# Kernel optimization log

Hardware: AMD Instinct MI355X
Metric: run time of the kernel (lower is better)

Reference implementation:

```python
import jax, jax.numpy as jnp
import numpy as np

B, S, D, H, DK, DV = 2, 2048, 1024, 16, 64, 64


def setup_inputs() -> dict:
    key = jax.random.key(0)
    ks = jax.random.split(key, 12)
    inp = {
        "query": jax.random.normal(ks[0], (B, S, D), jnp.float32),
        "key":   jax.random.normal(ks[1], (B, S, D), jnp.float32),
        "value": jax.random.normal(ks[2], (B, S, D), jnp.float32),
        # additive mask broadcast over per-head [B,S,S] scores (zeros = no masking)
        "mask":  jnp.zeros((S, S), jnp.float32),
        # stacked per-head projection params (math-equivalent to H separate Linears)
        "Wq": jax.random.normal(ks[3], (H, D, DK), jnp.float32) / np.sqrt(D),
        "bq": jax.random.normal(ks[4], (H, DK), jnp.float32) * 0.02,
        "Wk": jax.random.normal(ks[5], (H, D, DK), jnp.float32) / np.sqrt(D),
        "bk": jax.random.normal(ks[6], (H, DK), jnp.float32) * 0.02,
        "Wv": jax.random.normal(ks[7], (H, D, DV), jnp.float32) / np.sqrt(D),
        "bv": jax.random.normal(ks[8], (H, DV), jnp.float32) * 0.02,
        "Wo": jax.random.normal(ks[9], (H * DV, D), jnp.float32) / np.sqrt(H * DV),
        "bo": jax.random.normal(ks[10], (D,), jnp.float32) * 0.02,
    }
    return inp


def reference(query, key, value, mask, Wq, bq, Wk, bk, Wv, bv, Wo, bo):
    # per-head projections, vectorized over heads
    q = jnp.einsum("bsd,hdk->bhsk", query, Wq) + bq[None, :, None, :]
    k = jnp.einsum("bsd,hdk->bhsk", key, Wk) + bk[None, :, None, :]
    v = jnp.einsum("bsd,hdv->bhsv", value, Wv) + bv[None, :, None, :]
    # explicit QK^T softmax V, scale by sqrt(dim_k) (key.size(-1))
    scores = jnp.einsum("bhsk,bhtk->bhst", q, k) / jnp.sqrt(jnp.asarray(DK, q.dtype))
    scores = scores + mask  # broadcast [S,S] -> [B,H,S,S]
    attn = jax.nn.softmax(scores, axis=-1)
    out = jnp.einsum("bhst,bhtv->bhsv", attn, v)
    # concat heads along last dim: [B,S,H*DV]
    out = out.transpose(0, 2, 1, 3).reshape(B, S, H * DV)
    return out @ Wo + bo
```

## Files before the change

kernel.cpp:

```cpp
#include <hip/hip_runtime.h>
#include <stdint.h>

typedef __bf16 bf16;
typedef float f32x4 __attribute__((ext_vector_type(4)));
typedef __bf16 bf16x8 __attribute__((ext_vector_type(8)));
typedef __bf16 bf16x4 __attribute__((ext_vector_type(4)));

__device__ __forceinline__ void async_load16(const void* g, void* l) {
    __builtin_amdgcn_global_load_lds(
        (const __attribute__((address_space(1))) void*)g,
        (__attribute__((address_space(3))) void*)l, 16, 0, 0);
}

__global__ void detect_dtype(const unsigned short* __restrict__ q, int* __restrict__ flag) {
    __shared__ int cnt;
    if (threadIdx.x == 0) cnt = 0;
    __syncthreads();
    int c = 0;
    for (int i = threadIdx.x; i < 4096; i += 256) {
        int e = (q[i] >> 7) & 0xFF;
        if (e >= 0xC0) ++c;
    }
    atomicAdd(&cnt, c);
    __syncthreads();
    if (threadIdx.x == 0) { flag[0] = (cnt > 64) ? 1 : 0; flag[1] = 0; }
}

__global__ void prep(const void* __restrict__ qv, const void* __restrict__ vv,
                     const void* __restrict__ wq, const void* __restrict__ wk,
                     const void* __restrict__ wv, const void* __restrict__ wo,
                     const unsigned int* __restrict__ mask,
                     bf16* __restrict__ Xq, bf16* __restrict__ Xv,
                     bf16* __restrict__ WqT, bf16* __restrict__ WoT,
                     int* __restrict__ flag) {
    __shared__ bf16 t[32][33];
    const int f    = flag[0];
    const int task = blockIdx.z;
    const int bid  = blockIdx.x + 64 * blockIdx.y;

    if (task < 2) {
        const void* x = task ? vv : qv;
        bf16* o = task ? Xv : Xq;
        size_t i = ((size_t)bid * 256 + threadIdx.x) * 8;
        if (f) {
            f32x4 a = ((const f32x4*)x)[i / 4];
            f32x4 b = ((const f32x4*)x)[i / 4 + 1];
            bf16x8 v;
            for (int j = 0; j < 4; ++j) { v[j] = (bf16)a[j]; v[4 + j] = (bf16)b[j]; }
            *(bf16x8*)(o + i) = v;
        } else {
            *(bf16x8*)(o + i) = *(const bf16x8*)((const bf16*)x + i);
        }
    } else if (task < 5) {
        if (bid >= 1024) return;
        const void* in = (task == 2) ? wq : ((task == 3) ? wk : wv);
        int sub = bid >> 6, rem = bid & 63;
        int c0 = (rem & 1) * 32, r0 = (rem >> 1) * 32;
        int tx = threadIdx.x & 31, ty = threadIdx.x >> 5;
        size_t base = (size_t)sub * 65536;
        if (f) {
            const float* inF = (const float*)in;
            for (int i = 0; i < 32; i += 8)
                t[ty + i][tx] = (bf16)inF[base + (size_t)(r0 + ty + i) * 64 + (c0 + tx)];
        } else {
            const bf16* inB = (const bf16*)in;
            for (int i = 0; i < 32; i += 8)
                t[ty + i][tx] = inB[base + (size_t)(r0 + ty + i) * 64 + (c0 + tx)];
        }
        __syncthreads();
        bf16* o = WqT + ((size_t)(task - 2) * 16 + sub) * 65536;
        for (int i = 0; i < 32; i += 8)
            o[(size_t)(c0 + ty + i) * 1024 + (r0 + tx)] = t[tx][ty + i];
    } else if (task == 5) {
        if (bid >= 1024) return;
        int c0 = (bid & 31) * 32, r0 = (bid >> 5) * 32;
        int tx = threadIdx.x & 31, ty = threadIdx.x >> 5;
        if (f) {
            const float* inF = (const float*)wo;
            for (int i = 0; i < 32; i += 8)
                t[ty + i][tx] = (bf16)inF[(size_t)(r0 + ty + i) * 1024 + (c0 + tx)];
        } else {
            const bf16* inB = (const bf16*)wo;
            for (int i = 0; i < 32; i += 8)
                t[ty + i][tx] = inB[(size_t)(r0 + ty + i) * 1024 + (c0 + tx)];
        }
        __syncthreads();
        for (int i = 0; i < 32; i += 8)
            WoT[(size_t)(c0 + ty + i) * 1024 + (r0 + tx)] = t[tx][ty + i];
    } else {
        const long nvec = (f ? 4194304L : 2097152L) / 4;
        unsigned int acc = 0;
        long stride = 2048L * 256;
        for (long i = (long)bid * 256 + threadIdx.x; i < nvec; i += stride) {
            uint4 v = ((const uint4*)mask)[i];
            acc |= v.x | v.y | v.z | v.w;
        }
        if (acc) atomicOr(flag + 1, 1);
    }
}

__global__ __launch_bounds__(256, 3) void gemm_qkv(
    const bf16* __restrict__ Xq, const void* __restrict__ keyRaw,
    const bf16* __restrict__ Xv, const bf16* __restrict__ Bt,
    const void* __restrict__ b0, const void* __restrict__ b1, const void* __restrict__ b2,
    bf16* __restrict__ Qp, bf16* __restrict__ Kp, bf16* __restrict__ Vt,
    const int* __restrict__ flag) {
    __shared__ __attribute__((aligned(16))) unsigned char AsRaw[128 * 64 * 4];
    __shared__ __attribute__((aligned(16))) bf16 Bs[128 * 64];

    const int f = flag[0];
    const int K = 1024, N = 1024;
    const int z = blockIdx.z;
    const int af = (z == 1) ? f : 0;
    const void* Av   = (z == 0) ? (const void*)Xq : ((z == 1) ? keyRaw : (const void*)Xv);
    const void* bias = (z == 0) ? b0 : ((z == 1) ? b1 : b2);
    const bf16* B    = Bt + (size_t)z * 1024 * 1024;

    const int tid  = threadIdx.x;
    const int lane = tid & 63;
    const int w    = tid >> 6;
    const int quad = lane >> 4;
    const int mrow = lane & 15;
    const int m0 = blockIdx.y * 128;
    const int n0 = blockIdx.x * 128;
    const int wm = (w & 1) * 64;
    const int wn = (w >> 1) * 64;

    f32x4 acc[4][4] = {};

    for (int k0 = 0; k0 < K; k0 += 64) {
        if (af) {
            for (int it = 0; it < 8; ++it) {
                int ci  = it * 256 + tid;
                int row = ci >> 4, pc = ci & 15;
                int swz = ((row & 7) << 1) | ((row >> 3) & 1);
                int gc  = pc ^ swz;
                async_load16((const float*)Av + (size_t)(m0 + row) * K + k0 + gc * 4,
                             AsRaw + (size_t)(it * 256 + w * 64) * 16);
            }
        } else {
            for (int it = 0; it < 4; ++it) {
                int ci  = it * 256 + tid;
                int row = ci >> 3, pc = ci & 7;
                int gc  = pc ^ (row & 7);
                async_load16((const bf16*)Av + (size_t)(m0 + row) * K + k0 + gc * 8,
                             (bf16*)AsRaw + (size_t)(it * 256 + w * 64) * 8);
            }
        }
        for (int it = 0; it < 4; ++it) {
            int ci  = it * 256 + tid;
            int row = ci >> 3, pc = ci & 7;
            int gc  = pc ^ (row & 7);
            async_load16(B + (size_t)(n0 + row) * K + k0 + gc * 8,
                         Bs + (size_t)(it * 256 + w * 64) * 8);
        }
        __syncthreads();
        for (int kk = 0; kk < 2; ++kk) {
            bf16x8 afr[4], bfr[4];
            if (af) {
                const float* Asf = (const float*)AsRaw;
                for (int mi = 0; mi < 4; ++mi) {
                    int row = wm + mi * 16 + mrow;
                    int swz = ((row & 7) << 1) | ((row >> 3) & 1);
                    int lc  = (kk * 4 + quad) * 2;
                    f32x4 u0 = *(const f32x4*)(Asf + row * 64 + (lc ^ swz) * 4);
                    f32x4 u1 = *(const f32x4*)(Asf + row * 64 + ((lc + 1) ^ swz) * 4);
                    for (int j = 0; j < 4; ++j) {
                        afr[mi][j]     = (bf16)u0[j];
                        afr[mi][4 + j] = (bf16)u1[j];
                    }
                }
            } else {
                const bf16* Asb = (const bf16*)AsRaw;
                for (int mi = 0; mi < 4; ++mi) {
                    int row = wm + mi * 16 + mrow;
                    int pc  = (kk * 4 + quad) ^ (row & 7);
                    afr[mi] = *(const bf16x8*)(Asb + row * 64 + pc * 8);
                }
            }
            for (int ni = 0; ni < 4; ++ni) {
                int row = wn + ni * 16 + mrow;
                int pc  = (kk * 4 + quad) ^ (row & 7);
                bfr[ni] = *(const bf16x8*)(Bs + row * 64 + pc * 8);
            }
            for (int mi = 0; mi < 4; ++mi)
                for (int ni = 0; ni < 4; ++ni)
                    acc[mi][ni] = __builtin_amdgcn_mfma_f32_16x16x32_bf16(
                        afr[mi], bfr[ni], acc[mi][ni], 0, 0, 0);
        }
        __syncthreads();
    }

    const float scl = (z == 0) ? 0.18033688f : 1.0f;
    for (int ni = 0; ni < 4; ++ni) {
        int n    = n0 + wn + ni * 16 + mrow;
        float bv = f ? ((const float*)bias)[n] : (float)((const bf16*)bias)[n];
        for (int mi = 0; mi < 4; ++mi) {
            int mb = m0 + wm + mi * 16 + quad * 4;
            if (z == 2) {
                bf16x4 pk;
                for (int r = 0; r < 4; ++r) pk[r] = (bf16)(acc[mi][ni][r] + bv);
                *(bf16x4*)(Vt + (((size_t)(mb >> 11) * 1024 + n) << 11) + (mb & 2047)) = pk;
            } else {
                bf16* P = (z == 0) ? Qp : Kp;
                for (int r = 0; r < 4; ++r)
                    P[(size_t)(mb + r) * N + n] = (bf16)((acc[mi][ni][r] + bv) * scl);
            }
        }
    }
}

__global__ __launch_bounds__(256, 2) void gemm_out(
    const bf16* __restrict__ A, const bf16* __restrict__ Bt,
    const void* __restrict__ bias, void* __restrict__ Cout,
    const int* __restrict__ flag) {
    __shared__ __attribute__((aligned(16))) bf16 As[128 * 64];
    __shared__ __attribute__((aligned(16))) bf16 Bs[64 * 64];

    const int f = flag[0];
    const int K = 1024, N = 1024;
    const int tid  = threadIdx.x;
    const int lane = tid & 63;
    const int w    = tid >> 6;
    const int quad = lane >> 4;
    const int mrow = lane & 15;
    const int m0 = blockIdx.y * 128;
    const int n0 = blockIdx.x * 64;
    const int wm = (w & 1) * 64;
    const int wn = (w >> 1) * 32;

    f32x4 acc[4][2] = {};

    for (int k0 = 0; k0 < K; k0 += 64) {
        for (int it = 0; it < 4; ++it) {
            int ci  = it * 256 + tid;
            int row = ci >> 3, pc = ci & 7;
            int gc  = pc ^ (row & 7);
            async_load16(A + (size_t)(m0 + row) * K + k0 + gc * 8,
                         As + (size_t)(it * 256 + w * 64) * 8);
        }
        for (int it = 0; it < 2; ++it) {
            int ci  = it * 256 + tid;
            int row = ci >> 3, pc = ci & 7;
            int gc  = pc ^ (row & 7);
            async_load16(Bt + (size_t)(n0 + row) * K + k0 + gc * 8,
                         Bs + (size_t)(it * 256 + w * 64) * 8);
        }
        __syncthreads();
        for (int kk = 0; kk < 2; ++kk) {
            bf16x8 afr[4], bfr[2];
            for (int mi = 0; mi < 4; ++mi) {
                int row = wm + mi * 16 + mrow;
                int pc  = (kk * 4 + quad) ^ (row & 7);
                afr[mi] = *(const bf16x8*)(As + row * 64 + pc * 8);
            }
            for (int ni = 0; ni < 2; ++ni) {
                int row = wn + ni * 16 + mrow;
                int pc  = (kk * 4 + quad) ^ (row & 7);
                bfr[ni] = *(const bf16x8*)(Bs + row * 64 + pc * 8);
            }
            for (int mi = 0; mi < 4; ++mi)
                for (int ni = 0; ni < 2; ++ni)
                    acc[mi][ni] = __builtin_amdgcn_mfma_f32_16x16x32_bf16(
                        afr[mi], bfr[ni], acc[mi][ni], 0, 0, 0);
        }
        __syncthreads();
    }

    for (int ni = 0; ni < 2; ++ni) {
        int n    = n0 + wn + ni * 16 + mrow;
        float bv = f ? ((const float*)bias)[n] : (float)((const bf16*)bias)[n];
        for (int mi = 0; mi < 4; ++mi) {
            int mb = m0 + wm + mi * 16 + quad * 4;
            for (int r = 0; r < 4; ++r) {
                float val = acc[mi][ni][r] + bv;
                if (f) ((float*)Cout)[(size_t)(mb + r) * N + n] = val;
                else   ((bf16*)Cout)[(size_t)(mb + r) * N + n] = (bf16)val;
            }
        }
    }
}

__global__ __launch_bounds__(256, 2) void flash_attn(
    const bf16* __restrict__ Qp, const bf16* __restrict__ Kp,
    const bf16* __restrict__ Vt, const void* __restrict__ maskv,
    bf16* __restrict__ O, const int* __restrict__ flag) {
    __shared__ __attribute__((aligned(16))) bf16 Ks[2][4096];
    __shared__ __attribute__((aligned(16))) bf16 Vs[2][4096];
    __shared__ __attribute__((aligned(16))) bf16 Ps[128 * 72];

    const int f       = flag[0];
    const int useMask = flag[1];
    const int tid  = threadIdx.x;
    const int lane = tid & 63;
    const int w    = tid >> 6;
    const int quad = lane >> 4;
    const int c    = lane & 15;
    const int s0   = blockIdx.x * 128;
    const int h    = blockIdx.y;
    const int b    = blockIdx.z;

    const size_t qkBase = (size_t)b * 2048 * 1024 + h * 64;
    const size_t vtBase = ((size_t)b * 1024 + h * 64) * 2048;

    const int ci0 = tid, ci1 = 256 + tid;
    const int r0 = ci0 >> 3, g0 = (ci0 & 7) ^ (r0 & 7);
    const int r1 = ci1 >> 3, g1 = (ci1 & 7) ^ (r1 & 7);
    const bf16* kp0 = Kp + qkBase + (size_t)r0 * 1024 + g0 * 8;
    const bf16* kp1 = Kp + qkBase + (size_t)r1 * 1024 + g1 * 8;
    const bf16* vp0 = Vt + vtBase + (size_t)r0 * 2048 + g0 * 8;
    const bf16* vp1 = Vt + vtBase + (size_t)r1 * 2048 + g1 * 8;

#define STAGE(B_, T_) do {                                                             \
        async_load16(kp0 + (size_t)(T_) * 1024, &Ks[B_][(size_t)(w * 64) * 8]);        \
        async_load16(kp1 + (size_t)(T_) * 1024, &Ks[B_][(size_t)(256 + w * 64) * 8]);  \
        async_load16(vp0 + (T_),                &Vs[B_][(size_t)(w * 64) * 8]);        \
        async_load16(vp1 + (T_),                &Vs[B_][(size_t)(256 + w * 64) * 8]);  \
    } while (0)

    const bf16* kf0 = &Ks[0][c * 64 + ((0 + quad) ^ (c & 7)) * 8];
    const bf16* kf1 = &Ks[0][c * 64 + ((4 + quad) ^ (c & 7)) * 8];
    const bf16* vf0 = &Vs[0][c * 64 + ((0 + quad) ^ (c & 7)) * 8];
    const bf16* vf1 = &Vs[0][c * 64 + ((4 + quad) ^ (c & 7)) * 8];
    bf16*       pw0 = Ps + (w * 32 + c) * 72 + quad * 4;
    bf16*       pw1 = Ps + (w * 32 + 16 + c) * 72 + quad * 4;
    const bf16* pr0 = Ps + (w * 32 + c) * 72 + quad * 8;
    const bf16* pr1 = Ps + (w * 32 + 16 + c) * 72 + quad * 8;

    bf16x8 aq[2][2];
    for (int hh = 0; hh < 2; ++hh) {
        const bf16* qrow = Qp + qkBase + (size_t)(s0 + w * 32 + hh * 16 + c) * 1024;
        aq[hh][0] = *(const bf16x8*)(qrow + quad * 8);
        aq[hh][1] = *(const bf16x8*)(qrow + 32 + quad * 8);
    }

    f32x4 o_acc[2][4] = {};
    float l_s[2] = {0.f, 0.f};

    const size_t mb0 = (size_t)(s0 + w * 32 + c) * 2048;
    const size_t mb1 = (size_t)(s0 + w * 32 + 16 + c) * 2048;

#define FCOMP(IB_, T_) do {                                                              \
        f32x4 sc[2][4] = {};                                                             \
        _Pragma("unroll") for (int tt = 0; tt < 4; ++tt) {                               \
            bf16x8 ak0 = *(const bf16x8*)(kf0 + (IB_) * 4096 + tt * 1024);               \
            bf16x8 ak1 = *(const bf16x8*)(kf1 + (IB_) * 4096 + tt * 1024);               \
            sc[0][tt] = __builtin_amdgcn_mfma_f32_16x16x32_bf16(ak0, aq[0][0], sc[0][tt], 0, 0, 0); \
            sc[0][tt] = __builtin_amdgcn_mfma_f32_16x16x32_bf16(ak1, aq[0][1], sc[0][tt], 0, 0, 0); \
            sc[1][tt] = __builtin_amdgcn_mfma_f32_16x16x32_bf16(ak0, aq[1][0], sc[1][tt], 0, 0, 0); \
            sc[1][tt] = __builtin_amdgcn_mfma_f32_16x16x32_bf16(ak1, aq[1][1], sc[1][tt], 0, 0, 0); \
        }                                                                                \
        if (useMask) {                                                                   \
            _Pragma("unroll") for (int hh = 0; hh < 2; ++hh) {                           \
                const size_t mr = (hh ? mb1 : mb0) + (T_);                               \
                _Pragma("unroll") for (int tt = 0; tt < 4; ++tt) {                       \
                    if (f) {                                                             \
                        f32x4 mk = *(const f32x4*)((const float*)maskv + mr + tt * 16 + quad * 4); \
                        for (int r = 0; r < 4; ++r) sc[hh][tt][r] += mk[r] * 1.44269504f; \
                    } else {                                                             \
                        bf16x4 mk = *(const bf16x4*)((const bf16*)maskv + mr + tt * 16 + quad * 4); \
                        for (int r = 0; r < 4; ++r) sc[hh][tt][r] += (float)mk[r] * 1.44269504f; \
                    }                                                                    \
                }                                                                        \
            }                                                                            \
        }                                                                                \
        _Pragma("unroll") for (int hh = 0; hh < 2; ++hh) {                               \
            float rsum = 0.f;                                                            \
            bf16* pw = hh ? pw1 : pw0;                                                   \
            _Pragma("unroll") for (int tt = 0; tt < 4; ++tt) {                           \
                bf16x4 pk;                                                               \
                for (int r = 0; r < 4; ++r) {                                            \
                    float p = exp2f(sc[hh][tt][r]);                                      \
                    rsum += p;                                                           \
                    pk[r] = (bf16)p;                                                     \
                }                                                                        \
                *(bf16x4*)(pw + tt * 16) = pk;                                           \
            }                                                                            \
            l_s[hh] += rsum;                                                             \
        }                                                                                \
        _Pragma("unroll") for (int kk = 0; kk < 2; ++kk) {                               \
            bf16x8 ap0 = *(const bf16x8*)((kk ? pr0 + 32 : pr0));                        \
            bf16x8 ap1 = *(const bf16x8*)((kk ? pr1 + 32 : pr1));                        \
            const bf16* vfb = kk ? vf1 : vf0;                                            \
            _Pragma("unroll") for (int ni = 0; ni < 4; ++ni) {                           \
                bf16x8 bv = *(const bf16x8*)(vfb + (IB_) * 4096 + ni * 1024);            \
                o_acc[0][ni] = __builtin_amdgcn_mfma_f32_16x16x32_bf16(ap0, bv, o_acc[0][ni], 0, 0, 0); \
                o_acc[1][ni] = __builtin_amdgcn_mfma_f32_16x16x32_bf16(ap1, bv, o_acc[1][ni], 0, 0, 0); \
            }                                                                            \
        }                                                                                \
    } while (0)

    STAGE(0, 0);
    for (int t0 = 0; t0 < 2048; t0 += 128) {
        __syncthreads();
        STAGE(1, t0 + 64);
        FCOMP(0, t0);
        __syncthreads();
        if (t0 + 128 < 2048) STAGE(0, t0 + 128);
        FCOMP(1, t0 + 64);
    }
#undef STAGE
#undef FCOMP

    for (int hh = 0; hh < 2; ++hh) {
        float ls = l_s[hh];
        ls += __shfl_xor(ls, 16, 64);
        ls += __shfl_xor(ls, 32, 64);
        for (int r = 0; r < 4; ++r) {
            float lv   = __shfl(ls, quad * 4 + r, 64);
            float inv  = 1.0f / lv;
            size_t roff = (size_t)(b * 2048 + s0 + w * 32 + hh * 16 + quad * 4 + r) * 1024 + h * 64;
            for (int ni = 0; ni < 4; ++ni)
                O[roff + ni * 16 + c] = (bf16)(o_acc[hh][ni][r] * inv);
        }
    }
}

extern "C" void kernel_launch(void* const* d_in, const int* in_sizes, int n_in,
                              void* d_out, int out_size, void* d_ws, size_t ws_size,
                              hipStream_t stream) {
    bf16* ws = (bf16*)d_ws;
    (void)in_sizes; (void)n_in; (void)out_size; (void)ws_size;

    const size_t MM = 1024 * 1024;
    int*  flag = (int*)ws;
    bf16* WqT  = ws + 8;
    bf16* WoT  = WqT + 3 * MM;
    bf16* Qp   = WoT + MM;
    bf16* Kp   = Qp + 4 * MM;
    bf16* Xq   = Kp + 4 * MM;
    bf16* AO   = Xq;
    bf16* Xv   = (bf16*)d_out;
    bf16* Vt   = (bf16*)d_out + 4 * MM;

    detect_dtype<<<1, 256, 0, stream>>>((const unsigned short*)d_in[0], flag);

    prep<<<dim3(64, 32, 7), 256, 0, stream>>>(d_in[0], d_in[2], d_in[4], d_in[6],
                                              d_in[8], d_in[10],
                                              (const unsigned int*)d_in[3],
                                              Xq, Xv, WqT, WoT, flag);

    gemm_qkv<<<dim3(8, 32, 3), 256, 0, stream>>>(Xq, d_in[1], Xv, WqT,
                                                 d_in[5], d_in[7], d_in[9],
                                                 Qp, Kp, Vt, flag);

    flash_attn<<<dim3(16, 16, 2), 256, 0, stream>>>(Qp, Kp, Vt, d_in[3], AO, flag);

    gemm_out<<<dim3(16, 32, 1), 256, 0, stream>>>(AO, WoT, d_in[11], d_out, flag);
}
```

Measured before the change: 268.4 us.

## Keep softmax probabilities in registers via permlane swaps instead of LDS round-trip

Replaces the shared-memory staging of the P tile (write bf16 probabilities to LDS, then read them back in MFMA A-operand layout) with in-register repacking. The values are converted to packed bf16 pairs and shuffled across lanes with permlane32/permlane16 swaps. This removes LDS writes and reads plus the shared buffer, which cuts LDS traffic and footprint. It also wraps the MFMA sections in s_setprio to favour matrix issue across waves. The lane-permutation mapping must exactly match the MFMA operand layout, and it relies on gfx950 permlane swap instructions.

Result: slower. 274.4 us (+2.3%).

```diff
diff --git a/kernel.cpp b/kernel.cpp
--- a/kernel.cpp
+++ b/kernel.cpp
@@ -5,12 +5,33 @@
 typedef float f32x4 __attribute__((ext_vector_type(4)));
 typedef __bf16 bf16x8 __attribute__((ext_vector_type(8)));
 typedef __bf16 bf16x4 __attribute__((ext_vector_type(4)));
+typedef __bf16 bf16x2 __attribute__((ext_vector_type(2)));
+typedef unsigned u32x2 __attribute__((ext_vector_type(2)));
+typedef unsigned u32x4 __attribute__((ext_vector_type(4)));
 
 __device__ __forceinline__ void async_load16(const void* g, void* l) {
     __builtin_amdgcn_global_load_lds(
         (const __attribute__((address_space(1))) void*)g,
         (__attribute__((address_space(3))) void*)l, 16, 0, 0);
 }
+
+__device__ __forceinline__ unsigned pk2(float lo, float hi) {
+    bf16x2 t;
+    t[0] = (bf16)lo;
+    t[1] = (bf16)hi;
+    return __builtin_bit_cast(unsigned, t);
+}
+
+#if __has_builtin(__builtin_amdgcn_permlane32_swap)
+#define PLSWAP32(A_, B_) do { u32x2 _r = __builtin_amdgcn_permlane32_swap((A_), (B_), false, false); (A_) = _r[0]; (B_) = _r[1]; } while (0)
+#else
+#define PLSWAP32(A_, B_) asm("v_permlane32_swap_b32 %0, %1" : "+v"(A_), "+v"(B_))
+#endif
+#if __has_builtin(__builtin_amdgcn_permlane16_swap)
+#define PLSWAP16(A_, B_) do { u32x2 _r = __builtin_amdgcn_permlane16_swap((A_), (B_), false, false); (A_) = _r[0]; (B_) = _r[1]; } while (0)
+#else
+#define PLSWAP16(A_, B_) asm("v_permlane16_swap_b32 %0, %1" : "+v"(A_), "+v"(B_))
+#endif
 
 __global__ void detect_dtype(const unsigned short* __restrict__ q, int* __restrict__ flag) {
     __shared__ int cnt;
@@ -287,7 +308,6 @@
     bf16* __restrict__ O, const int* __restrict__ flag) {
     __shared__ __attribute__((aligned(16))) bf16 Ks[2][4096];
     __shared__ __attribute__((aligned(16))) bf16 Vs[2][4096];
-    __shared__ __attribute__((aligned(16))) bf16 Ps[128 * 72];
 
     const int f       = flag[0];
     const int useMask = flag[1];
@@ -322,10 +342,6 @@
     const bf16* kf1 = &Ks[0][c * 64 + ((4 + quad) ^ (c & 7)) * 8];
     const bf16* vf0 = &Vs[0][c * 64 + ((0 + quad) ^ (c & 7)) * 8];
     const bf16* vf1 = &Vs[0][c * 64 + ((4 + quad) ^ (c & 7)) * 8];
-    bf16*       pw0 = Ps + (w * 32 + c) * 72 + quad * 4;
-    bf16*       pw1 = Ps + (w * 32 + 16 + c) * 72 + quad * 4;
-    const bf16* pr0 = Ps + (w * 32 + c) * 72 + quad * 8;
-    const bf16* pr1 = Ps + (w * 32 + 16 + c) * 72 + quad * 8;
 
     bf16x8 aq[2][2];
     for (int hh = 0; hh < 2; ++hh) {
@@ -342,6 +358,7 @@
 
 #define FCOMP(IB_, T_) do {                                                              \
         f32x4 sc[2][4] = {};                                                             \
+        __builtin_amdgcn_s_setprio(1);                                                   \
         _Pragma("unroll") for (int tt = 0; tt < 4; ++tt) {                               \
             bf16x8 ak0 = *(const bf16x8*)(kf0 + (IB_) * 4096 + tt * 1024);               \
             bf16x8 ak1 = *(const bf16x8*)(kf1 + (IB_) * 4096 + tt * 1024);               \
@@ -350,6 +367,7 @@
             sc[1][tt] = __builtin_amdgcn_mfma_f32_16x16x32_bf16(ak0, aq[1][0], sc[1][tt], 0, 0, 0); \
             sc[1][tt] = __builtin_amdgcn_mfma_f32_16x16x32_bf16(ak1, aq[1][1], sc[1][tt], 0, 0, 0); \
         }                                                                                \
+        __builtin_amdgcn_s_setprio(0);                                                   \
         if (useMask) {                                                                   \
             _Pragma("unroll") for (int hh = 0; hh < 2; ++hh) {                           \
                 const size_t mr = (hh ? mb1 : mb0) + (T_);                               \
@@ -364,30 +382,41 @@
                 }                                                                        \
             }                                                                            \
         }                                                                                \
+        unsigned Wp[2][4][2];                                                            \
         _Pragma("unroll") for (int hh = 0; hh < 2; ++hh) {                               \
             float rsum = 0.f;                                                            \
-            bf16* pw = hh ? pw1 : pw0;                                                   \
             _Pragma("unroll") for (int tt = 0; tt < 4; ++tt) {                           \
-                bf16x4 pk;                                                               \
-                for (int r = 0; r < 4; ++r) {                                            \
-                    float p = exp2f(sc[hh][tt][r]);                                      \
-                    rsum += p;                                                           \
-                    pk[r] = (bf16)p;                                                     \
-                }                                                                        \
-                *(bf16x4*)(pw + tt * 16) = pk;                                           \
+                float p0 = exp2f(sc[hh][tt][0]), p1 = exp2f(sc[hh][tt][1]);              \
+                float p2 = exp2f(sc[hh][tt][2]), p3 = exp2f(sc[hh][tt][3]);              \
+                rsum += (p0 + p1) + (p2 + p3);                                           \
+                Wp[hh][tt][0] = pk2(p0, p1);                                             \
+                Wp[hh][tt][1] = pk2(p2, p3);                                             \
             }                                                                            \
             l_s[hh] += rsum;                                                             \
         }                                                                                \
+        bf16x8 ap[2][2];                                                                 \
         _Pragma("unroll") for (int kk = 0; kk < 2; ++kk) {                               \
-            bf16x8 ap0 = *(const bf16x8*)((kk ? pr0 + 32 : pr0));                        \
-            bf16x8 ap1 = *(const bf16x8*)((kk ? pr1 + 32 : pr1));                        \
-            const bf16* vfb = kk ? vf1 : vf0;                                            \
-            _Pragma("unroll") for (int ni = 0; ni < 4; ++ni) {                           \
-                bf16x8 bv = *(const bf16x8*)(vfb + (IB_) * 4096 + ni * 1024);            \
-                o_acc[0][ni] = __builtin_amdgcn_mfma_f32_16x16x32_bf16(ap0, bv, o_acc[0][ni], 0, 0, 0); \
-                o_acc[1][ni] = __builtin_amdgcn_mfma_f32_16x16x32_bf16(ap1, bv, o_acc[1][ni], 0, 0, 0); \
+            _Pragma("unroll") for (int hh = 0; hh < 2; ++hh) {                           \
+                unsigned a0 = Wp[hh][2 * kk][0], b0v = Wp[hh][2 * kk + 1][0];            \
+                unsigned a1 = Wp[hh][2 * kk][1], b1v = Wp[hh][2 * kk + 1][1];            \
+                PLSWAP32(a0, b0v);                                                       \
+                PLSWAP16(a0, b0v);                                                       \
+                PLSWAP32(a1, b1v);                                                       \
+                PLSWAP16(a1, b1v);                                                       \
+                u32x4 uv; uv[0] = a0; uv[1] = a1; uv[2] = b0v; uv[3] = b1v;              \
+                ap[kk][hh] = __builtin_bit_cast(bf16x8, uv);                             \
             }                                                                            \
         }                                                                                \
+        __builtin_amdgcn_s_setprio(1);                                                   \
+        _Pragma("unroll") for (int kk = 0; kk < 2; ++kk) {                               \
+            const bf16* vfb = (kk ? vf1 : vf0) + (IB_) * 4096;                           \
+            _Pragma("unroll") for (int ni = 0; ni < 4; ++ni) {                           \
+                bf16x8 bv = *(const bf16x8*)(vfb + ni * 1024);                           \
+                o_acc[0][ni] = __builtin_amdgcn_mfma_f32_16x16x32_bf16(ap[kk][0], bv, o_acc[0][ni], 0, 0, 0); \
+                o_acc[1][ni] = __builtin_amdgcn_mfma_f32_16x16x32_bf16(ap[kk][1], bv, o_acc[1][ni], 0, 0, 0); \
+            }                                                                            \
+        }                                                                                \
+        __builtin_amdgcn_s_setprio(0);                                                   \
     } while (0)
 
     STAGE(0, 0);
```
